# Optimization experiments

Measured on AMD Instinct MI355X. Metric: run time of the kernel, lower is better.

Reference implementation:

```python
import jax, jax.numpy as jnp
import numpy as np

WS = 8   # window_size
SS = 4   # shift_size
NH = 4   # num_heads


def _window_partition(x, w):
    B, H, W, C = x.shape
    x = x.reshape(B, H // w, w, W // w, w, C).transpose(0, 1, 3, 2, 4, 5)
    return x.reshape(-1, w, w, C)


def _window_reverse(win, w, H, W):
    B = win.shape[0] // ((H // w) * (W // w))
    x = win.reshape(B, H // w, W // w, w, w, -1).transpose(0, 1, 3, 2, 4, 5)
    return x.reshape(B, H, W, -1)


def _rel_pos_index(w):
    coords = np.stack(np.meshgrid(np.arange(w), np.arange(w), indexing='ij'))  # (2,w,w)
    cf = coords.reshape(2, -1)
    rel = cf[:, :, None] - cf[:, None, :]          # (2,N,N)
    rel = rel.transpose(1, 2, 0)                   # (N,N,2)
    rel[:, :, 0] += w - 1
    rel[:, :, 1] += w - 1
    rel[:, :, 0] *= 2 * w - 1
    return rel.sum(-1)                             # (N,N) int


def _attn_mask(Hp, Wp, w, ss):
    if ss == 0:
        return None
    img = np.zeros((1, Hp, Wp, 1), np.float32)
    slices = (slice(0, -w), slice(-w, -ss), slice(-ss, None))
    cnt = 0
    for h in slices:
        for ww in slices:
            img[:, h, ww, :] = cnt
            cnt += 1
    mw = img.reshape(1, Hp // w, w, Wp // w, w, 1).transpose(0, 1, 3, 2, 4, 5).reshape(-1, w * w)
    m = mw[:, None, :] - mw[:, :, None]
    return np.where(m != 0, -100.0, 0.0).astype(np.float32)  # (nW,N,N)


def _ln(x, g, b, eps=1e-5):
    mu = x.mean(-1, keepdims=True)
    var = ((x - mu) ** 2).mean(-1, keepdims=True)
    return (x - mu) * jax.lax.rsqrt(var + eps) * g + b


def setup_inputs() -> dict:
    key = jax.random.key(0)
    ks = jax.random.split(key, 8)
    B, H, W, C = 4, 256, 256, 128
    hid = 4 * C
    s = 0.02
    return {
        'x': jax.random.normal(ks[0], (B, H * W, C), jnp.float32),
        'norm1_g': jnp.ones((C,), jnp.float32),
        'norm1_b': jnp.zeros((C,), jnp.float32),
        'qkv_w': jax.random.normal(ks[1], (3 * C, C), jnp.float32) * s,
        'qkv_b': jnp.zeros((3 * C,), jnp.float32),
        'rpb_table': jax.random.normal(ks[2], ((2 * WS - 1) ** 2, NH), jnp.float32) * s,
        'proj_w': jax.random.normal(ks[3], (C, C), jnp.float32) * s,
        'proj_b': jnp.zeros((C,), jnp.float32),
        'norm2_g': jnp.ones((C,), jnp.float32),
        'norm2_b': jnp.zeros((C,), jnp.float32),
        'fc1_w': jax.random.normal(ks[4], (hid, C), jnp.float32) * s,
        'fc1_b': jnp.zeros((hid,), jnp.float32),
        'fc2_w': jax.random.normal(ks[5], (C, hid), jnp.float32) * s,
        'fc2_b': jnp.zeros((C,), jnp.float32),
        'H': H,
        'W': W,
    }


def reference(x, norm1_g, norm1_b, qkv_w, qkv_b, rpb_table, proj_w, proj_b,
              norm2_g, norm2_b, fc1_w, fc1_b, fc2_w, fc2_b, H, W):
    B, L, C = x.shape
    hd = C // NH
    scale = hd ** -0.5
    N = WS * WS

    shortcut = x
    h = _ln(x, norm1_g, norm1_b).reshape(B, H, W, C)

    pad_r = (WS - W % WS) % WS
    pad_b = (WS - H % WS) % WS
    if pad_r > 0 or pad_b > 0:
        h = jnp.pad(h, ((0, 0), (0, pad_b), (0, pad_r), (0, 0)))
    Hp, Wp = H + pad_b, W + pad_r

    if SS > 0:
        h = jnp.roll(h, (-SS, -SS), axis=(1, 2))

    win = _window_partition(h, WS).reshape(-1, N, C)   # (B_,N,C)
    B_ = win.shape[0]

    qkv = (win @ qkv_w.T + qkv_b).reshape(B_, N, 3, NH, hd).transpose(2, 0, 3, 1, 4)
    q, k, v = qkv[0] * scale, qkv[1], qkv[2]           # (B_,NH,N,hd)

    attn = jnp.einsum('whnd,whmd->whnm', q, k)         # (B_,NH,N,N)
    rpi = _rel_pos_index(WS).reshape(-1)
    bias = rpb_table[rpi].reshape(N, N, NH).transpose(2, 0, 1)
    attn = attn + bias[None]

    mask = _attn_mask(Hp, Wp, WS, SS)
    if mask is not None:
        nW = mask.shape[0]
        attn = attn.reshape(B_ // nW, nW, NH, N, N) + jnp.asarray(mask)[None, :, None]
        attn = attn.reshape(B_, NH, N, N)

    attn = jax.nn.softmax(attn, axis=-1)
    out = jnp.einsum('whnm,whmd->whnd', attn, v).transpose(0, 2, 1, 3).reshape(B_, N, C)
    out = out @ proj_w.T + proj_b

    out = _window_reverse(out.reshape(-1, WS, WS, C), WS, Hp, Wp)
    if SS > 0:
        out = jnp.roll(out, (SS, SS), axis=(1, 2))
    if pad_r > 0 or pad_b > 0:
        out = out[:, :H, :W, :]
    x = shortcut + out.reshape(B, H * W, C)

    y = _ln(x, norm2_g, norm2_b)
    y = jax.nn.gelu(y @ fc1_w.T + fc1_b, approximate=False) @ fc2_w.T + fc2_b
    return x + y
```

## Files before the change

kernel.cpp:

```cpp
#include <hip/hip_runtime.h>
#include <hip/hip_bf16.h>

typedef unsigned short u16;
typedef unsigned int u32;
typedef __attribute__((ext_vector_type(8))) short bf16x8;
typedef __attribute__((ext_vector_type(4))) float f32x4;

__device__ __forceinline__ u32 fbits(float f) { union { float f; u32 u; } a; a.f = f; return a.u; }
__device__ __forceinline__ u16 f2bf(float f) {
    u32 u = fbits(f);
    return (u16)((u + 0x7FFFu + ((u >> 16) & 1u)) >> 16);
}
__device__ __forceinline__ u16 bfr(float f) { return (u16)((fbits(f) + 0x8000u) >> 16); }
__device__ __forceinline__ u32 pk2(float lo, float hi) {
    return __builtin_amdgcn_perm(fbits(hi) + 0x8000u, fbits(lo) + 0x8000u, 0x07060302u);
}
__device__ __forceinline__ float bf2f(u16 b) {
    union { u32 u; float f; } a; a.u = ((u32)b) << 16; return a.f;
}

#define MFMA(a, b, c) __builtin_amdgcn_mfma_f32_16x16x32_bf16(a, b, c, 0, 0, 0)

__device__ __forceinline__ void gload16(const u16* g, u16* l) {
    __builtin_amdgcn_global_load_lds(
        (const __attribute__((address_space(1))) void*)g,
        (__attribute__((address_space(3))) void*)l, 16, 0, 0);
}

__global__ void swin_prep_kernel(const float* __restrict__ qkv_w, const float* __restrict__ proj_w,
                                 const float* __restrict__ fc1_w, const float* __restrict__ fc2_w,
                                 const float* __restrict__ rpb, u16* __restrict__ wout,
                                 float* __restrict__ bias_lane)
{
    int idx = blockIdx.x * 256 + threadIdx.x;
    if (idx < 49152) wout[idx] = f2bf(qkv_w[idx]);
    else if (idx < 81920) {
        int j = idx - 49152;
        int tile = j >> 9, lane = (j >> 3) & 63, e = j & 7;
        int nt = tile >> 2, ks = tile & 3;
        wout[idx] = f2bf(proj_w[(nt * 16 + (lane & 15)) * 128 + ks * 32 + (lane >> 4) * 8 + e]);
    } else if (idx < 212992) {
        int j = idx - 81920;
        int chunk = j >> 13, rest = j & 8191;
        int tile = rest >> 9, lane = (rest >> 3) & 63, e = rest & 7;
        float v;
        if (tile < 8) {
            int n2 = tile >> 2, ks = tile & 3;
            v = fc1_w[(chunk * 32 + n2 * 16 + (lane & 15)) * 128 + ks * 32 + (lane >> 4) * 8 + e];
        } else {
            int nt = tile - 8;
            v = fc2_w[(nt * 16 + (lane & 15)) * 512 + chunk * 32 + (lane >> 4) * 8 + e];
        }
        wout[idx] = f2bf(v);
    } else {
        int t = idx - 212992;
        int r = t & 3, lane = (t >> 2) & 63, nt = (t >> 8) & 3, mt = (t >> 10) & 3;
        int h = (t >> 12) & 3, v = (t >> 14) & 3;
        int i = mt * 16 + ((lane >> 4) << 2) + r;
        int j = nt * 16 + (lane & 15);
        int ri = i >> 3, ci = i & 7, rj = j >> 3, cj = j & 7;
        int rpi = (ri - rj + 7) * 15 + (ci - cj + 7);
        float bv = rpb[rpi * 4 + h];
        int vh = v >> 1, vw = v & 1;
        int regi = (vh ? (ri < 4 ? 1 : 2) : 0) * 3 + (vw ? (ci < 4 ? 1 : 2) : 0);
        int regj = (vh ? (rj < 4 ? 1 : 2) : 0) * 3 + (vw ? (cj < 4 ? 1 : 2) : 0);
        if (regi != regj) bv -= 100.0f;
        bias_lane[t] = bv;
    }
}

__global__ __launch_bounds__(512, 4) void swin_attn_kernel(
    const float* __restrict__ x, const float* __restrict__ g1, const float* __restrict__ b1,
    const float* __restrict__ qkvb, const u16* __restrict__ qkvw,
    const float* __restrict__ bias_lane, u16* __restrict__ attn_out)
{
    __shared__ __align__(16) u16 ldsX[64 * 132];
    __shared__ __align__(16) u16 ldsQK[17408];
    __shared__ __align__(16) u16 vT[128][72];
    __shared__ float sb[640];

    int tid = threadIdx.x;
    int wid = blockIdx.x;
    int bb_ = wid >> 10, wh = (wid >> 5) & 31, ww = wid & 31;

    for (int i = tid; i < 640; i += 512) {
        float v;
        if (i < 128) v = g1[i];
        else if (i < 256) v = b1[i - 128];
        else v = qkvb[i - 256];
        sb[i] = v;
    }

    int trow = tid >> 3, seg = tid & 7;
    int rn = trow >> 3, cn = trow & 7;
    int srow = (wh * 8 + rn + 4) & 255;
    int scol = (ww * 8 + cn + 4) & 255;
    long grow = (long)bb_ * 65536 + srow * 256 + scol;
    const float4* xrow = (const float4*)(x + grow * 128 + seg * 16);
    float4 xv[4];
    #pragma unroll
    for (int i = 0; i < 4; ++i) xv[i] = xrow[i];
    __syncthreads();

    float s1 = 0.0f, s2 = 0.0f;
    #pragma unroll
    for (int i = 0; i < 4; ++i) {
        float4 v = xv[i];
        s1 += v.x + v.y + v.z + v.w;
        s2 += v.x * v.x + v.y * v.y + v.z * v.z + v.w * v.w;
    }
    #pragma unroll
    for (int off = 1; off < 8; off <<= 1) { s1 += __shfl_xor(s1, off); s2 += __shfl_xor(s2, off); }
    float mu = s1 * 0.0078125f;
    float rstd = rsqrtf(s2 * 0.0078125f - mu * mu + 1e-5f);
    {
        u32 pk[8];
        #pragma unroll
        for (int i = 0; i < 4; ++i) {
            float vv[4] = {xv[i].x, xv[i].y, xv[i].z, xv[i].w};
            float y0, y1, y2, y3;
            {
                int c = seg * 16 + i * 4;
                y0 = (vv[0] - mu) * rstd * sb[c + 0] + sb[128 + c + 0];
                y1 = (vv[1] - mu) * rstd * sb[c + 1] + sb[128 + c + 1];
                y2 = (vv[2] - mu) * rstd * sb[c + 2] + sb[128 + c + 2];
                y3 = (vv[3] - mu) * rstd * sb[c + 3] + sb[128 + c + 3];
            }
            pk[i * 2]     = pk2(y0, y1);
            pk[i * 2 + 1] = pk2(y2, y3);
        }
        *(uint4*)&ldsX[trow * 132 + seg * 16] = *(uint4*)&pk[0];
        *(uint4*)&ldsX[trow * 132 + seg * 16 + 8] = *(uint4*)&pk[4];
    }
    __syncthreads();

    int wave = tid >> 6, lane = tid & 63, l15 = lane & 15, lg = lane >> 4;
    int mrow = lg * 4;
    bf16x8 afr[4][4];
    #pragma unroll
    for (int mt = 0; mt < 4; ++mt)
        #pragma unroll
        for (int ks = 0; ks < 4; ++ks)
            afr[mt][ks] = *(const bf16x8*)&ldsX[(mt * 16 + l15) * 132 + ks * 32 + lg * 8];
    #pragma unroll 1
    for (int nn = 0; nn < 3; ++nn) {
        int nt = wave * 3 + nn;
        int n = nt * 16 + l15;
        const u16* wp = qkvw + n * 128 + lg * 8;
        bf16x8 bfr_[4];
        #pragma unroll
        for (int ks = 0; ks < 4; ++ks) bfr_[ks] = *(const bf16x8*)(wp + ks * 32);
        f32x4 acc[4];
        #pragma unroll
        for (int mt = 0; mt < 4; ++mt) acc[mt] = (f32x4){0.0f, 0.0f, 0.0f, 0.0f};
        #pragma unroll
        for (int ks = 0; ks < 4; ++ks)
            #pragma unroll
            for (int mt = 0; mt < 4; ++mt)
                acc[mt] = MFMA(afr[mt][ks], bfr_[ks], acc[mt]);
        float bias = sb[256 + n];
        if (n < 128) {
            #pragma unroll
            for (int mt = 0; mt < 4; ++mt)
                #pragma unroll
                for (int r = 0; r < 4; ++r)
                    ldsQK[(mt * 16 + mrow + r) * 132 + n] = bfr(acc[mt][r] + bias);
        } else if (n < 256) {
            #pragma unroll
            for (int mt = 0; mt < 4; ++mt)
                #pragma unroll
                for (int r = 0; r < 4; ++r)
                    ldsQK[8448 + (mt * 16 + mrow + r) * 132 + (n - 128)] = bfr(acc[mt][r] + bias);
        } else {
            #pragma unroll
            for (int mt = 0; mt < 4; ++mt) {
                uint2 pv;
                pv.x = pk2(acc[mt][0] + bias, acc[mt][1] + bias);
                pv.y = pk2(acc[mt][2] + bias, acc[mt][3] + bias);
                *(uint2*)&vT[n - 256][mt * 16 + mrow] = pv;
            }
        }
    }
    __syncthreads();

    int h = wave >> 1, half = wave & 1;
    int v4 = ((wh == 31) ? 2 : 0) | ((ww == 31) ? 1 : 0);
    const float4* blp = (const float4*)bias_lane;
    bf16x8 bk[4];
    #pragma unroll
    for (int nt = 0; nt < 4; ++nt)
        bk[nt] = *(const bf16x8*)&ldsQK[8448 + (nt * 16 + l15) * 132 + h * 32 + lg * 8];
    f32x4 sS[2][4];
    #pragma unroll
    for (int m2 = 0; m2 < 2; ++m2) {
        int mt = half * 2 + m2;
        bf16x8 aq = *(const bf16x8*)&ldsQK[(mt * 16 + l15) * 132 + h * 32 + lg * 8];
        #pragma unroll
        for (int nt = 0; nt < 4; ++nt) {
            f32x4 z = (f32x4){0.0f, 0.0f, 0.0f, 0.0f};
            z = MFMA(aq, bk[nt], z);
            float4 bl = blp[((v4 * 4 + h) * 16 + mt * 4 + nt) * 64 + lane];
            sS[m2][nt][0] = z[0] * 0.1767766952966369f + bl.x;
            sS[m2][nt][1] = z[1] * 0.1767766952966369f + bl.y;
            sS[m2][nt][2] = z[2] * 0.1767766952966369f + bl.z;
            sS[m2][nt][3] = z[3] * 0.1767766952966369f + bl.w;
        }
    }
    float rinv[2][4];
    #pragma unroll
    for (int m2 = 0; m2 < 2; ++m2) {
        #pragma unroll
        for (int r = 0; r < 4; ++r) {
            float mx = fmaxf(fmaxf(sS[m2][0][r], sS[m2][1][r]), fmaxf(sS[m2][2][r], sS[m2][3][r]));
            #pragma unroll
            for (int off = 1; off < 16; off <<= 1) mx = fmaxf(mx, __shfl_xor(mx, off));
            float sum = 0.0f;
            #pragma unroll
            for (int nt = 0; nt < 4; ++nt) {
                float p = __expf(sS[m2][nt][r] - mx);
                sS[m2][nt][r] = p;
                sum += p;
            }
            #pragma unroll
            for (int off = 1; off < 16; off <<= 1) sum += __shfl_xor(sum, off);
            rinv[m2][r] = __builtin_amdgcn_rcpf(sum);
        }
    }
    __syncthreads();
    #pragma unroll
    for (int m2 = 0; m2 < 2; ++m2) {
        int mt = half * 2 + m2;
        #pragma unroll
        for (int nt = 0; nt < 4; ++nt)
            #pragma unroll
            for (int r = 0; r < 4; ++r)
                ldsQK[h * 4352 + (mt * 16 + mrow + r) * 68 + nt * 16 + l15] = bfr(sS[m2][nt][r]);
    }
    __syncthreads();

    f32x4 o[2][2];
    #pragma unroll
    for (int m2 = 0; m2 < 2; ++m2)
        #pragma unroll
        for (int np = 0; np < 2; ++np) o[m2][np] = (f32x4){0.0f, 0.0f, 0.0f, 0.0f};
    #pragma unroll
    for (int kt = 0; kt < 2; ++kt) {
        bf16x8 pa[2];
        #pragma unroll
        for (int m2 = 0; m2 < 2; ++m2) {
            int mt = half * 2 + m2;
            pa[m2] = *(const bf16x8*)&ldsQK[h * 4352 + (mt * 16 + l15) * 68 + kt * 32 + lg * 8];
        }
        #pragma unroll
        for (int np = 0; np < 2; ++np) {
            bf16x8 bv = *(const bf16x8*)&vT[h * 32 + np * 16 + l15][kt * 32 + lg * 8];
            #pragma unroll
            for (int m2 = 0; m2 < 2; ++m2)
                o[m2][np] = MFMA(pa[m2], bv, o[m2][np]);
        }
    }
    #pragma unroll
    for (int m2 = 0; m2 < 2; ++m2) {
        int mt = half * 2 + m2;
        #pragma unroll
        for (int np = 0; np < 2; ++np)
            #pragma unroll
            for (int r = 0; r < 4; ++r)
                ldsX[(mt * 16 + mrow + r) * 132 + h * 32 + np * 16 + l15] = bfr(o[m2][np][r] * rinv[m2][r]);
    }
    __syncthreads();
    u16* op = attn_out + grow * 128 + seg * 16;
    *(uint4*)op = *(const uint4*)&ldsX[trow * 132 + seg * 16];
    *(uint4*)(op + 8) = *(const uint4*)&ldsX[trow * 132 + seg * 16 + 8];
}

__global__ __launch_bounds__(256, 3) void swin_mlp_kernel(
    const u16* __restrict__ attn, const float* __restrict__ x,
    const u16* __restrict__ projws, const u16* __restrict__ wms,
    const float* __restrict__ projb, const float* __restrict__ g2, const float* __restrict__ b2,
    const float* __restrict__ f1b, const float* __restrict__ f2b, float* __restrict__ out)
{
    __shared__ __align__(16) u16 wbuf[2][8192];
    __shared__ __align__(16) u16 sbuf[4][1152];

    int tid = threadIdx.x;
    int wave = tid >> 6, lane = tid & 63, l15 = lane & 15, lg = lane >> 4;
    long wbase = (long)blockIdx.x * 128 + wave * 32;

    {
        const u16* src = wms + wave * 2048 + lane * 8;
        u16* dst = &wbuf[0][wave * 2048];
        #pragma unroll
        for (int i = 0; i < 4; ++i)
            gload16(src + i * 512, dst + i * 512);
    }

    const u16* arow = attn + (wbase + l15) * 128 + lg * 8;
    bf16x8 aat[2][4];
    #pragma unroll
    for (int ks = 0; ks < 4; ++ks) {
        aat[0][ks] = *(const bf16x8*)(arow + ks * 32);
        aat[1][ks] = *(const bf16x8*)(arow + 2048 + ks * 32);
    }

    f32x4 pacc[2][8];
    #pragma unroll
    for (int nt = 0; nt < 8; ++nt) {
        const u16* wp = projws + nt * 2048 + lane * 8;
        pacc[0][nt] = (f32x4){0.0f, 0.0f, 0.0f, 0.0f};
        pacc[1][nt] = (f32x4){0.0f, 0.0f, 0.0f, 0.0f};
        #pragma unroll
        for (int ks = 0; ks < 4; ++ks) {
            bf16x8 bw = *(const bf16x8*)(wp + ks * 512);
            pacc[0][nt] = MFMA(aat[0][ks], bw, pacc[0][nt]);
            pacc[1][nt] = MFMA(aat[1][ks], bw, pacc[1][nt]);
        }
    }

    #pragma unroll
    for (int nt = 0; nt < 8; ++nt) {
        float pb = projb[nt * 16 + l15];
        #pragma unroll
        for (int mt = 0; mt < 2; ++mt)
            #pragma unroll
            for (int r = 0; r < 4; ++r)
                pacc[mt][nt][r] += x[(wbase + mt * 16 + lg * 4 + r) * 128 + nt * 16 + l15] + pb;
    }
    float mu[2][4], rstd[2][4];
    #pragma unroll
    for (int mt = 0; mt < 2; ++mt)
        #pragma unroll
        for (int r = 0; r < 4; ++r) {
            float a = 0.0f, bq = 0.0f;
            #pragma unroll
            for (int nt = 0; nt < 8; ++nt) { a += pacc[mt][nt][r]; bq += pacc[mt][nt][r] * pacc[mt][nt][r]; }
            #pragma unroll
            for (int off = 1; off < 16; off <<= 1) { a += __shfl_xor(a, off); bq += __shfl_xor(bq, off); }
            mu[mt][r] = a * 0.0078125f;
            rstd[mt][r] = rsqrtf(bq * 0.0078125f - mu[mt][r] * mu[mt][r] + 1e-5f);
        }
    u16* hb = (u16*)sbuf[wave];
    bf16x8 ay[2][4];
    #pragma unroll
    for (int p = 0; p < 4; ++p) {
        #pragma unroll
        for (int mt = 0; mt < 2; ++mt)
            #pragma unroll
            for (int n2 = 0; n2 < 2; ++n2) {
                int c = p * 32 + n2 * 16 + l15;
                float gg = g2[c], bb = b2[c];
                int nt = p * 2 + n2;
                #pragma unroll
                for (int r = 0; r < 4; ++r)
                    hb[(mt * 16 + lg * 4 + r) * 36 + n2 * 16 + l15] =
                        bfr((pacc[mt][nt][r] - mu[mt][r]) * rstd[mt][r] * gg + bb);
            }
        __builtin_amdgcn_sched_barrier(0);
        ay[0][p] = *(const bf16x8*)&hb[l15 * 36 + lg * 8];
        ay[1][p] = *(const bf16x8*)&hb[(16 + l15) * 36 + lg * 8];
        __builtin_amdgcn_sched_barrier(0);
    }
    #pragma unroll
    for (int nt = 0; nt < 8; ++nt) {
        float fb = f2b[nt * 16 + l15];
        #pragma unroll
        for (int mt = 0; mt < 2; ++mt)
            #pragma unroll
            for (int r = 0; r < 4; ++r)
                pacc[mt][nt][r] += fb;
    }
    __syncthreads();

    #pragma unroll 1
    for (int cc = 0; cc < 16; ++cc) {
        int cur = cc & 1;
        if (cc < 15) {
            const u16* src = wms + (cc + 1) * 8192 + wave * 2048 + lane * 8;
            u16* dst = &wbuf[cur ^ 1][wave * 2048];
            #pragma unroll
            for (int i = 0; i < 4; ++i)
                gload16(src + i * 512, dst + i * 512);
        }
        f32x4 h[2][2];
        h[0][0] = h[0][1] = h[1][0] = h[1][1] = (f32x4){0.0f, 0.0f, 0.0f, 0.0f};
        #pragma unroll
        for (int n2 = 0; n2 < 2; ++n2)
            #pragma unroll
            for (int ks = 0; ks < 4; ++ks) {
                bf16x8 bw = *(const bf16x8*)&wbuf[cur][(n2 * 4 + ks) * 512 + lane * 8];
                h[0][n2] = MFMA(ay[0][ks], bw, h[0][n2]);
                h[1][n2] = MFMA(ay[1][ks], bw, h[1][n2]);
            }
        #pragma unroll
        for (int n2 = 0; n2 < 2; ++n2) {
            float fb = f1b[cc * 32 + n2 * 16 + l15];
            #pragma unroll
            for (int mt = 0; mt < 2; ++mt)
                #pragma unroll
                for (int r = 0; r < 4; ++r) {
                    float t = h[mt][n2][r] + fb;
                    float ge = t * __builtin_amdgcn_rcpf(1.0f + exp2f(t * -2.4553418f));
                    hb[(mt * 16 + lg * 4 + r) * 36 + n2 * 16 + l15] = bfr(ge);
                }
        }
        __builtin_amdgcn_sched_barrier(0);
        bf16x8 ah0 = *(const bf16x8*)&hb[l15 * 36 + lg * 8];
        bf16x8 ah1 = *(const bf16x8*)&hb[(16 + l15) * 36 + lg * 8];
        __builtin_amdgcn_sched_barrier(0);
        #pragma unroll
        for (int nt = 0; nt < 8; ++nt) {
            bf16x8 bw = *(const bf16x8*)&wbuf[cur][(8 + nt) * 512 + lane * 8];
            pacc[0][nt] = MFMA(ah0, bw, pacc[0][nt]);
            pacc[1][nt] = MFMA(ah1, bw, pacc[1][nt]);
        }
        __syncthreads();
    }
    #pragma unroll
    for (int nt = 0; nt < 8; ++nt)
        #pragma unroll
        for (int mt = 0; mt < 2; ++mt)
            #pragma unroll
            for (int r = 0; r < 4; ++r)
                out[(wbase + mt * 16 + lg * 4 + r) * 128 + nt * 16 + l15] = pacc[mt][nt][r];
}

extern "C" void kernel_launch(void* const* d_in, const int* in_sizes, int n_in,
                              void* d_out, int out_size, void* d_ws, size_t ws_size,
                              hipStream_t stream)
{
    const float* x     = (const float*)d_in[0];
    const float* n1g   = (const float*)d_in[1];
    const float* n1b   = (const float*)d_in[2];
    const float* qkvw  = (const float*)d_in[3];
    const float* qkvb  = (const float*)d_in[4];
    const float* rpb   = (const float*)d_in[5];
    const float* projw = (const float*)d_in[6];
    const float* projb = (const float*)d_in[7];
    const float* n2g   = (const float*)d_in[8];
    const float* n2b   = (const float*)d_in[9];
    const float* f1w   = (const float*)d_in[10];
    const float* f1b   = (const float*)d_in[11];
    const float* f2w   = (const float*)d_in[12];
    const float* f2b   = (const float*)d_in[13];

    char* ws = (char*)d_ws;
    u16* attn_buf = (u16*)ws;
    u16* wb = (u16*)(ws + 67108864);
    float* bias_lane = (float*)(ws + 67108864 + 425984);
    u16* qkvwb  = wb;
    u16* projws = wb + 49152;
    u16* wms    = wb + 81920;

    swin_prep_kernel<<<1088, 256, 0, stream>>>(qkvw, projw, f1w, f2w, rpb, wb, bias_lane);
    swin_attn_kernel<<<4096, 512, 0, stream>>>(x, n1g, n1b, qkvb, qkvwb, bias_lane, attn_buf);
    swin_mlp_kernel<<<2048, 256, 0, stream>>>(attn_buf, x, projws, wms,
                                              projb, n2g, n2b, f1b, f2b, (float*)d_out);
}
```

Before: 261.4 us.

## Software-pipeline fused MLP loop: peel first fc1 chunk, overlap next fc1 with fc2

Measured after the change: 263.4 us. No clear change (+0.8%).

```diff
diff --git a/kernel.cpp b/kernel.cpp
--- a/kernel.cpp
+++ b/kernel.cpp
@@ -371,29 +371,27 @@
     }
     __syncthreads();
 
-    #pragma unroll 1
-    for (int cc = 0; cc < 16; ++cc) {
-        int cur = cc & 1;
-        if (cc < 15) {
-            const u16* src = wms + (cc + 1) * 8192 + wave * 2048 + lane * 8;
-            u16* dst = &wbuf[cur ^ 1][wave * 2048];
-            #pragma unroll
-            for (int i = 0; i < 4; ++i)
-                gload16(src + i * 512, dst + i * 512);
-        }
+    {
+        const u16* src = wms + 8192 + wave * 2048 + lane * 8;
+        u16* dst = &wbuf[1][wave * 2048];
+        #pragma unroll
+        for (int i = 0; i < 4; ++i)
+            gload16(src + i * 512, dst + i * 512);
+    }
+    {
         f32x4 h[2][2];
         h[0][0] = h[0][1] = h[1][0] = h[1][1] = (f32x4){0.0f, 0.0f, 0.0f, 0.0f};
         #pragma unroll
         for (int n2 = 0; n2 < 2; ++n2)
             #pragma unroll
             for (int ks = 0; ks < 4; ++ks) {
-                bf16x8 bw = *(const bf16x8*)&wbuf[cur][(n2 * 4 + ks) * 512 + lane * 8];
+                bf16x8 bw = *(const bf16x8*)&wbuf[0][(n2 * 4 + ks) * 512 + lane * 8];
                 h[0][n2] = MFMA(ay[0][ks], bw, h[0][n2]);
                 h[1][n2] = MFMA(ay[1][ks], bw, h[1][n2]);
             }
         #pragma unroll
         for (int n2 = 0; n2 < 2; ++n2) {
-            float fb = f1b[cc * 32 + n2 * 16 + l15];
+            float fb = f1b[n2 * 16 + l15];
             #pragma unroll
             for (int mt = 0; mt < 2; ++mt)
                 #pragma unroll
@@ -403,17 +401,51 @@
                     hb[(mt * 16 + lg * 4 + r) * 36 + n2 * 16 + l15] = bfr(ge);
                 }
         }
-        __builtin_amdgcn_sched_barrier(0);
+    }
+
+    #pragma unroll 1
+    for (int cc = 0; cc < 16; ++cc) {
+        int cur = cc & 1;
         bf16x8 ah0 = *(const bf16x8*)&hb[l15 * 36 + lg * 8];
         bf16x8 ah1 = *(const bf16x8*)&hb[(16 + l15) * 36 + lg * 8];
-        __builtin_amdgcn_sched_barrier(0);
         #pragma unroll
         for (int nt = 0; nt < 8; ++nt) {
             bf16x8 bw = *(const bf16x8*)&wbuf[cur][(8 + nt) * 512 + lane * 8];
             pacc[0][nt] = MFMA(ah0, bw, pacc[0][nt]);
             pacc[1][nt] = MFMA(ah1, bw, pacc[1][nt]);
         }
-        __syncthreads();
+        if (cc < 15) {
+            __syncthreads();
+            if (cc < 14) {
+                const u16* src = wms + (cc + 2) * 8192 + wave * 2048 + lane * 8;
+                u16* dst = &wbuf[cur][wave * 2048];
+                #pragma unroll
+                for (int i = 0; i < 4; ++i)
+                    gload16(src + i * 512, dst + i * 512);
+            }
+            f32x4 h[2][2];
+            h[0][0] = h[0][1] = h[1][0] = h[1][1] = (f32x4){0.0f, 0.0f, 0.0f, 0.0f};
+            #pragma unroll
+            for (int n2 = 0; n2 < 2; ++n2)
+                #pragma unroll
+                for (int ks = 0; ks < 4; ++ks) {
+                    bf16x8 bw = *(const bf16x8*)&wbuf[cur ^ 1][(n2 * 4 + ks) * 512 + lane * 8];
+                    h[0][n2] = MFMA(ay[0][ks], bw, h[0][n2]);
+                    h[1][n2] = MFMA(ay[1][ks], bw, h[1][n2]);
+                }
+            #pragma unroll
+            for (int n2 = 0; n2 < 2; ++n2) {
+                float fb = f1b[(cc + 1) * 32 + n2 * 16 + l15];
+                #pragma unroll
+                for (int mt = 0; mt < 2; ++mt)
+                    #pragma unroll
+                    for (int r = 0; r < 4; ++r) {
+                        float t = h[mt][n2][r] + fb;
+                        float ge = t * __builtin_amdgcn_rcpf(1.0f + exp2f(t * -2.4553418f));
+                        hb[(mt * 16 + lg * 4 + r) * 36 + n2 * 16 + l15] = bfr(ge);
+                    }
+            }
+        }
     }
     #pragma unroll
     for (int nt = 0; nt < 8; ++nt)
```
